# Kernel optimization log

Measured on AMD Instinct MI355X. Metric: run time of the kernel, lower is better.

## Reference

```python
import jax, jax.numpy as jnp
import numpy as np

N_NODES = 100000
N_EDGES = 1600000
HIDDEN = 128
ETYPE_DIM = 16
N_ETYPES = 512
TEMP = 1.0
EPS = 1e-8


def setup_inputs() -> dict:
    key = jax.random.key(0)
    ks = jax.random.split(key, 9)
    d_in = HIDDEN * 2 + ETYPE_DIM  # 272
    return {
        "x": jax.random.normal(ks[0], (N_NODES, HIDDEN), dtype=jnp.float32),
        "edge_index": jax.random.randint(ks[1], (2, N_EDGES), 0, N_NODES),
        "edge_type": jax.random.randint(ks[2], (N_EDGES,), 0, N_ETYPES),
        "u": jax.random.uniform(ks[3], (N_EDGES,), dtype=jnp.float32),
        "etype_emb": jax.random.normal(ks[4], (N_ETYPES, ETYPE_DIM), dtype=jnp.float32),
        "W1": jax.random.normal(ks[5], (d_in, HIDDEN), dtype=jnp.float32) / np.sqrt(d_in),
        "b1": jnp.zeros((HIDDEN,), dtype=jnp.float32),
        "W2": jax.random.normal(ks[6], (HIDDEN, 1), dtype=jnp.float32) / np.sqrt(HIDDEN),
        "b2": jnp.zeros((1,), dtype=jnp.float32),
    }


def reference(x, edge_index, edge_type, u, etype_emb, W1, b1, W2, b2):
    src, dst = edge_index[0], edge_index[1]
    # gather src/dst node embeddings + edge-type embedding, concat -> [E, 2H+D]
    h = jnp.concatenate([x[src], x[dst], etype_emb[edge_type]], axis=-1)
    h = jax.nn.relu(h @ W1 + b1)           # [E, H]
    logits = (h @ W2 + b2).reshape(-1)      # [E]
    # straight-through Gumbel-sigmoid
    g = jnp.log(u + EPS) - jnp.log(1.0 - u + EPS)
    y = jax.nn.sigmoid((logits + g) / max(TEMP, 1e-6))
    y_hard = (y > 0.5).astype(y.dtype)
    y_st = jax.lax.stop_gradient(y_hard - y) + y
    return jnp.stack([logits, y, y_st])  # [3, E]
```

## Files before the change

kernel.cpp:

```cpp
#include <hip/hip_runtime.h>
#include <hip/hip_bf16.h>
#include <math.h>

#define HIDDEN 128
#define EPS_G 1e-8f

__global__ __launch_bounds__(256) void etype_proj_kernel(
    const float* __restrict__ ee, const float* __restrict__ W1,
    const float* __restrict__ b1, float* __restrict__ PetB, int n_etypes)
{
    int gid = blockIdx.x * 256 + threadIdx.x;
    int t = gid >> 7;
    int c = gid & 127;
    if (t >= n_etypes) return;
    float acc = b1[c];
    #pragma unroll
    for (int k = 0; k < 16; ++k)
        acc = fmaf(ee[t * 16 + k], W1[(256 + k) * 128 + c], acc);
    PetB[t * 128 + c] = acc;
}

#define BM 64
#define BK 32
#define BNN 256
#define ASTR 68

__global__ __launch_bounds__(256) void node_proj_kernel(
    const float* __restrict__ x, const float* __restrict__ W1,
    float* __restrict__ P, int n_nodes)
{
    __shared__ float As[BK * ASTR];
    __shared__ float Bs[BK * BNN];

    const int tid = threadIdx.x;
    const int m0  = blockIdx.x * BM;
    const int tm  = tid >> 5;
    const int tn  = tid & 31;

    float acc[8][8];
    #pragma unroll
    for (int i = 0; i < 8; ++i)
        #pragma unroll
        for (int j = 0; j < 8; ++j) acc[i][j] = 0.f;

    for (int kc = 0; kc < 128; kc += BK) {
        #pragma unroll
        for (int i = 0; i < 2; ++i) {
            int l   = tid + i * 256;
            int row = l >> 3;
            int k4  = (l & 7) << 2;
            int gr  = m0 + row;
            if (gr >= n_nodes) gr = n_nodes - 1;
            float4 v = *(const float4*)(x + (size_t)gr * 128 + kc + k4);
            As[(k4 + 0) * ASTR + row] = v.x;
            As[(k4 + 1) * ASTR + row] = v.y;
            As[(k4 + 2) * ASTR + row] = v.z;
            As[(k4 + 3) * ASTR + row] = v.w;
        }
        #pragma unroll
        for (int i = 0; i < 8; ++i) {
            int l   = tid + i * 256;
            int row = l >> 6;
            int c4  = (l & 63) << 2;
            const float* sp = (c4 < 128)
                ? (W1 + (size_t)(kc + row) * 128 + c4)
                : (W1 + (size_t)(128 + kc + row) * 128 + (c4 - 128));
            *(float4*)&Bs[row * BNN + c4] = *(const float4*)sp;
        }
        __syncthreads();

        #pragma unroll 4
        for (int kk = 0; kk < BK; ++kk) {
            float4 a0  = *(const float4*)&As[kk * ASTR + tm * 8];
            float4 a1  = *(const float4*)&As[kk * ASTR + tm * 8 + 4];
            float4 b0  = *(const float4*)&Bs[kk * BNN + tn * 4];
            float4 b1v = *(const float4*)&Bs[kk * BNN + 128 + tn * 4];
            float a[8] = {a0.x, a0.y, a0.z, a0.w, a1.x, a1.y, a1.z, a1.w};
            #pragma unroll
            for (int i = 0; i < 8; ++i) {
                acc[i][0] = fmaf(a[i], b0.x,  acc[i][0]);
                acc[i][1] = fmaf(a[i], b0.y,  acc[i][1]);
                acc[i][2] = fmaf(a[i], b0.z,  acc[i][2]);
                acc[i][3] = fmaf(a[i], b0.w,  acc[i][3]);
                acc[i][4] = fmaf(a[i], b1v.x, acc[i][4]);
                acc[i][5] = fmaf(a[i], b1v.y, acc[i][5]);
                acc[i][6] = fmaf(a[i], b1v.z, acc[i][6]);
                acc[i][7] = fmaf(a[i], b1v.w, acc[i][7]);
            }
        }
        __syncthreads();
    }

    #pragma unroll
    for (int i = 0; i < 8; ++i) {
        int gr = m0 + tm * 8 + i;
        if (gr < n_nodes) {
            float4 w0 = make_float4(acc[i][0], acc[i][1], acc[i][2], acc[i][3]);
            float4 w1 = make_float4(acc[i][4], acc[i][5], acc[i][6], acc[i][7]);
            *(float4*)(P + (size_t)gr * 256 + tn * 4)       = w0;
            *(float4*)(P + (size_t)gr * 256 + 128 + tn * 4) = w1;
        }
    }
}

__global__ __launch_bounds__(256) void edge_kernel(
    const int* __restrict__ ei, const int* __restrict__ et,
    const float* __restrict__ u, const float* __restrict__ P,
    const float* __restrict__ PetB, const float* __restrict__ W2,
    const float* __restrict__ b2, float* __restrict__ out, int E)
{
    int gtid = blockIdx.x * 256 + threadIdx.x;
    int e = gtid >> 4;
    int l = gtid & 15;
    if (e >= E) return;

    int src = ei[e];
    int dst = ei[E + e];
    int t   = et[e];
    float uu = u[e];

    const float4* ps = (const float4*)(P + (size_t)src * 256);
    const float4* pd = (const float4*)(P + (size_t)dst * 256 + 128);
    const float4* pe = (const float4*)(PetB + (size_t)t * 128);
    const float4* w2 = (const float4*)W2;

    float partial = 0.f;
    #pragma unroll
    for (int j = 0; j < 2; ++j) {
        int idx = l * 2 + j;
        float4 a = ps[idx];
        float4 b = pd[idx];
        float4 c = pe[idx];
        float4 w = w2[idx];
        float h0 = fmaxf(a.x + b.x + c.x, 0.f);
        float h1 = fmaxf(a.y + b.y + c.y, 0.f);
        float h2 = fmaxf(a.z + b.z + c.z, 0.f);
        float h3 = fmaxf(a.w + b.w + c.w, 0.f);
        partial = fmaf(h0, w.x, partial);
        partial = fmaf(h1, w.y, partial);
        partial = fmaf(h2, w.z, partial);
        partial = fmaf(h3, w.w, partial);
    }
    partial += __shfl_xor(partial, 1);
    partial += __shfl_xor(partial, 2);
    partial += __shfl_xor(partial, 4);
    partial += __shfl_xor(partial, 8);

    if (l == 0) {
        float logit = partial + b2[0];
        float g  = logf(uu + EPS_G) - logf(1.f - uu + EPS_G);
        float z  = logit + g;
        float yv = 1.f / (1.f + expf(-z));
        float yh = yv > 0.5f ? 1.f : 0.f;
        float yst = (yh - yv) + yv;
        out[e]         = logit;
        out[E + e]     = yv;
        out[2 * E + e] = yst;
    }
}

__global__ __launch_bounds__(256) void edge_direct_kernel(
    const float* __restrict__ x, const int* __restrict__ ei,
    const int* __restrict__ et, const float* __restrict__ u,
    const float* __restrict__ ee, const float* __restrict__ W1,
    const float* __restrict__ b1, const float* __restrict__ W2,
    const float* __restrict__ b2, float* __restrict__ out, int E)
{
    int wid  = (blockIdx.x * 256 + threadIdx.x) >> 6;
    int lane = threadIdx.x & 63;
    if (wid >= E) return;
    int src = ei[wid], dst = ei[E + wid], t = et[wid];
    int c0 = lane * 2;
    float acc0 = b1[c0], acc1 = b1[c0 + 1];
    for (int k = 0; k < 128; ++k) {
        float xs = x[(size_t)src * 128 + k];
        acc0 = fmaf(xs, W1[k * 128 + c0], acc0);
        acc1 = fmaf(xs, W1[k * 128 + c0 + 1], acc1);
    }
    for (int k = 0; k < 128; ++k) {
        float xd = x[(size_t)dst * 128 + k];
        acc0 = fmaf(xd, W1[(128 + k) * 128 + c0], acc0);
        acc1 = fmaf(xd, W1[(128 + k) * 128 + c0 + 1], acc1);
    }
    for (int k = 0; k < 16; ++k) {
        float ev = ee[t * 16 + k];
        acc0 = fmaf(ev, W1[(256 + k) * 128 + c0], acc0);
        acc1 = fmaf(ev, W1[(256 + k) * 128 + c0 + 1], acc1);
    }
    float partial = fmaxf(acc0, 0.f) * W2[c0] + fmaxf(acc1, 0.f) * W2[c0 + 1];
    #pragma unroll
    for (int off = 1; off < 64; off <<= 1) partial += __shfl_xor(partial, off);
    if (lane == 0) {
        float logit = partial + b2[0];
        float uu = u[wid];
        float g  = logf(uu + EPS_G) - logf(1.f - uu + EPS_G);
        float z  = logit + g;
        float yv = 1.f / (1.f + expf(-z));
        float yh = yv > 0.5f ? 1.f : 0.f;
        float yst = (yh - yv) + yv;
        out[wid]         = logit;
        out[E + wid]     = yv;
        out[2 * E + wid] = yst;
    }
}

extern "C" void kernel_launch(void* const* d_in, const int* in_sizes, int n_in,
                              void* d_out, int out_size, void* d_ws, size_t ws_size,
                              hipStream_t stream)
{
    const float* x   = (const float*)d_in[0];
    const int*   ei  = (const int*)d_in[1];
    const int*   et  = (const int*)d_in[2];
    const float* u   = (const float*)d_in[3];
    const float* ee  = (const float*)d_in[4];
    const float* W1  = (const float*)d_in[5];
    const float* b1  = (const float*)d_in[6];
    const float* W2  = (const float*)d_in[7];
    const float* b2  = (const float*)d_in[8];
    float* out = (float*)d_out;

    const int n_nodes  = in_sizes[0] / HIDDEN;
    const int E        = in_sizes[2];
    const int n_etypes = in_sizes[4] / 16;

    const size_t needP   = (size_t)n_nodes * 256 * sizeof(float);
    const size_t needPet = (size_t)n_etypes * 128 * sizeof(float);

    if (ws_size >= needP + needPet) {
        float* P    = (float*)d_ws;
        float* PetB = (float*)((char*)d_ws + needP);

        hipLaunchKernelGGL(etype_proj_kernel,
                           dim3((n_etypes * 128 + 255) / 256), dim3(256), 0, stream,
                           ee, W1, b1, PetB, n_etypes);
        hipLaunchKernelGGL(node_proj_kernel,
                           dim3((n_nodes + BM - 1) / BM), dim3(256), 0, stream,
                           x, W1, P, n_nodes);
        hipLaunchKernelGGL(edge_kernel,
                           dim3((int)(((size_t)E * 16 + 255) / 256)), dim3(256), 0, stream,
                           ei, et, u, P, PetB, W2, b2, out, E);
    } else {
        hipLaunchKernelGGL(edge_direct_kernel,
                           dim3((E + 3) / 4), dim3(256), 0, stream,
                           x, ei, et, u, ee, W1, b1, W2, b2, out, E);
    }
}
```

Before: 417.1 us.

## Add node projection kernel with full W1 in LDS and lane-broadcast x operands

Adds a node projection kernel that uses 1024-thread blocks. Each block loads the whole 128x256 slice of W1 into 128 KB of dynamic LDS once, and each wave holds 8 x rows in registers, broadcasting values with readlane instead of staging x through shared memory. The goal is to remove the repeated per-k-chunk W1 tile reloads and the syncthreads between chunks in the node GEMM. In exchange, each block must stage 128 KB of W1 per 128 rows, occupancy is one block per CU, and the scalar readlane broadcasts may limit FMA throughput. The old kernel remains as a fallback if the LDS attribute cannot be set.

```diff
diff --git a/kernel.cpp b/kernel.cpp
--- a/kernel.cpp
+++ b/kernel.cpp
@@ -4,6 +4,10 @@
 
 #define HIDDEN 128
 #define EPS_G 1e-8f
+
+__device__ __forceinline__ float rdlane(float v, int lane) {
+    return __int_as_float(__builtin_amdgcn_readlane(__float_as_int(v), lane));
+}
 
 __global__ __launch_bounds__(256) void etype_proj_kernel(
     const float* __restrict__ ee, const float* __restrict__ W1,
@@ -20,6 +24,75 @@
     PetB[t * 128 + c] = acc;
 }
 
+__global__ __launch_bounds__(1024, 1) void node_proj_big_kernel(
+    const float* __restrict__ x, const float* __restrict__ W1,
+    float* __restrict__ P, int n_nodes)
+{
+    extern __shared__ float Bs[];
+
+    const int tid  = threadIdx.x;
+    const int lane = tid & 63;
+    const int wv   = tid >> 6;
+    const int m0   = blockIdx.x * 128;
+    const int r0   = m0 + wv * 8;
+    const int nm1  = n_nodes - 1;
+    const int c0   = lane * 4;
+
+    #pragma unroll
+    for (int i = 0; i < 32; ++i) {
+        int l   = tid + i * 1024;
+        int k   = l >> 6;
+        int c4  = (l & 63) << 2;
+        const float* sp = (c4 < 128)
+            ? (W1 + (size_t)k * 128 + c4)
+            : (W1 + (size_t)(128 + k) * 128 + (c4 - 128));
+        *(float4*)&Bs[(size_t)k * 256 + c4] = *(const float4*)sp;
+    }
+
+    float xr[8][2];
+    #pragma unroll
+    for (int r = 0; r < 8; ++r) {
+        int gr = r0 + r;
+        if (gr > nm1) gr = nm1;
+        float2 v = *(const float2*)(x + (size_t)gr * 128 + lane * 2);
+        xr[r][0] = v.x;
+        xr[r][1] = v.y;
+    }
+
+    float acc[8][4];
+    #pragma unroll
+    for (int r = 0; r < 8; ++r)
+        #pragma unroll
+        for (int c = 0; c < 4; ++c) acc[r][c] = 0.f;
+
+    __syncthreads();
+
+    for (int k2 = 0; k2 < 64; ++k2) {
+        #pragma unroll
+        for (int j = 0; j < 2; ++j) {
+            const int k = (k2 << 1) | j;
+            float4 bv = *(const float4*)&Bs[(size_t)k * 256 + c0];
+            #pragma unroll
+            for (int r = 0; r < 8; ++r) {
+                float a = rdlane(xr[r][j], k2);
+                acc[r][0] = fmaf(a, bv.x, acc[r][0]);
+                acc[r][1] = fmaf(a, bv.y, acc[r][1]);
+                acc[r][2] = fmaf(a, bv.z, acc[r][2]);
+                acc[r][3] = fmaf(a, bv.w, acc[r][3]);
+            }
+        }
+    }
+
+    #pragma unroll
+    for (int r = 0; r < 8; ++r) {
+        int gr = r0 + r;
+        if (gr < n_nodes) {
+            float4 w = make_float4(acc[r][0], acc[r][1], acc[r][2], acc[r][3]);
+            *(float4*)(P + (size_t)gr * 256 + c0) = w;
+        }
+    }
+}
+
 #define BM 64
 #define BK 32
 #define BNN 256
@@ -30,7 +103,7 @@
     float* __restrict__ P, int n_nodes)
 {
     __shared__ float As[BK * ASTR];
-    __shared__ float Bs[BK * BNN];
+    __shared__ float Bs2[BK * BNN];
 
     const int tid = threadIdx.x;
     const int m0  = blockIdx.x * BM;
@@ -65,7 +138,7 @@
             const float* sp = (c4 < 128)
                 ? (W1 + (size_t)(kc + row) * 128 + c4)
                 : (W1 + (size_t)(128 + kc + row) * 128 + (c4 - 128));
-            *(float4*)&Bs[row * BNN + c4] = *(const float4*)sp;
+            *(float4*)&Bs2[row * BNN + c4] = *(const float4*)sp;
         }
         __syncthreads();
 
@@ -73,8 +146,8 @@
         for (int kk = 0; kk < BK; ++kk) {
             float4 a0  = *(const float4*)&As[kk * ASTR + tm * 8];
             float4 a1  = *(const float4*)&As[kk * ASTR + tm * 8 + 4];
-            float4 b0  = *(const float4*)&Bs[kk * BNN + tn * 4];
-            float4 b1v = *(const float4*)&Bs[kk * BNN + 128 + tn * 4];
+            float4 b0  = *(const float4*)&Bs2[kk * BNN + tn * 4];
+            float4 b1v = *(const float4*)&Bs2[kk * BNN + 128 + tn * 4];
             float a[8] = {a0.x, a0.y, a0.z, a0.w, a1.x, a1.y, a1.z, a1.w};
             #pragma unroll
             for (int i = 0; i < 8; ++i) {
@@ -225,6 +298,7 @@
 
     const size_t needP   = (size_t)n_nodes * 256 * sizeof(float);
     const size_t needPet = (size_t)n_etypes * 128 * sizeof(float);
+    const int    LDS_BIG = 128 * 256 * 4;
 
     if (ws_size >= needP + needPet) {
         float* P    = (float*)d_ws;
@@ -233,9 +307,21 @@
         hipLaunchKernelGGL(etype_proj_kernel,
                            dim3((n_etypes * 128 + 255) / 256), dim3(256), 0, stream,
                            ee, W1, b1, PetB, n_etypes);
-        hipLaunchKernelGGL(node_proj_kernel,
-                           dim3((n_nodes + BM - 1) / BM), dim3(256), 0, stream,
-                           x, W1, P, n_nodes);
+
+        hipError_t rc = hipFuncSetAttribute(
+            (const void*)node_proj_big_kernel,
+            hipFuncAttributeMaxDynamicSharedMemorySize, LDS_BIG);
+
+        if (rc == hipSuccess) {
+            hipLaunchKernelGGL(node_proj_big_kernel,
+                               dim3((n_nodes + 127) / 128), dim3(1024), LDS_BIG,
+                               stream, x, W1, P, n_nodes);
+        } else {
+            hipLaunchKernelGGL(node_proj_kernel,
+                               dim3((n_nodes + 63) / 64), dim3(256), 0, stream,
+                               x, W1, P, n_nodes);
+        }
+
         hipLaunchKernelGGL(edge_kernel,
                            dim3((int)(((size_t)E * 16 + 255) / 256)), dim3(256), 0, stream,
                            ei, et, u, P, PetB, W2, b2, out, E);
```

After: 491.8 us. 17.9% more time.
